# Kernel tuning notes

Measured on AMD Instinct MI355X. Metric: run time of the kernel, lower is better.

Reference implementation:

```python
import jax, jax.numpy as jnp
import numpy as np

D_MODEL = 1024
N_HEADS = 16
D_LATENT = 64
LN_EPS = 1e-5


def setup_inputs() -> dict:
    key = jax.random.key(0)
    ks = jax.random.split(key, 9)
    dm, h, dl = D_MODEL, N_HEADS, D_LATENT
    hd = h * dl
    # xavier_uniform with gain=0.1: limit = 0.1 * sqrt(6/(fan_in+fan_out))
    def xavier(k, fan_in, fan_out):
        lim = 0.1 * np.sqrt(6.0 / (fan_in + fan_out))
        return jax.random.uniform(k, (fan_in, fan_out), jnp.float32, -lim, lim)
    return {
        "x": jax.random.normal(ks[0], (4, 2048, dm), jnp.float32),
        "ln_g": jnp.ones((dm,), jnp.float32),
        "ln_b": jnp.zeros((dm,), jnp.float32),
        "wq": xavier(ks[1], dm, hd), "bq": jnp.zeros((hd,), jnp.float32),
        "wk": xavier(ks[2], dm, hd), "bk": jnp.zeros((hd,), jnp.float32),
        "wv": xavier(ks[3], dm, hd), "bv": jnp.zeros((hd,), jnp.float32),
        "wo": xavier(ks[4], hd, dm), "bo": jnp.zeros((dm,), jnp.float32),
    }


def reference(x, ln_g, ln_b, wq, bq, wk, bk, wv, bv, wo, bo):
    b, s, dm = x.shape
    h, dl = N_HEADS, D_LATENT
    # context = raw x (bound before LayerNorm in the torch code)
    context = x
    mu = jnp.mean(x, axis=-1, keepdims=True)
    var = jnp.var(x, axis=-1, keepdims=True)
    xn = (x - mu) * jax.lax.rsqrt(var + LN_EPS) * ln_g + ln_b
    q = (xn @ wq + bq).reshape(b, s, h, dl).transpose(0, 2, 1, 3)          # b h s d
    k = (context @ wk + bk).reshape(b, -1, h, dl).transpose(0, 2, 1, 3)    # b h t d
    v = (context @ wv + bv).reshape(b, -1, h, dl).transpose(0, 2, 1, 3)
    scores = jnp.einsum("bhsd,bhtd->bhst", q, k) / jnp.sqrt(jnp.float32(dl))
    attn = jax.nn.softmax(scores.astype(jnp.float32), axis=-1)
    # dropout omitted (eval mode / deterministic reference)
    out = jnp.einsum("bhst,bhtd->bhsd", attn, v)
    out = out.transpose(0, 2, 1, 3).reshape(b, s, h * dl)
    return out @ wo + bo
```

## Files before the change

### kernel.cpp

```cpp
#include <hip/hip_runtime.h>
#include <cstdint>

typedef __attribute__((ext_vector_type(8))) __bf16 bf16x8;
typedef __attribute__((ext_vector_type(8))) unsigned short u16x8;
typedef __attribute__((ext_vector_type(4))) unsigned short u16x4;
typedef __attribute__((ext_vector_type(4))) float f32x4;
typedef __attribute__((ext_vector_type(2))) unsigned int u32x2;
typedef __attribute__((ext_vector_type(4))) unsigned int u32x4;

__device__ inline unsigned short f2bf(float f) {
  return __builtin_bit_cast(unsigned short, (__bf16)f);
}

__device__ inline void llds16(const void* g, void* l) {
  __builtin_amdgcn_global_load_lds((const uint32_t*)g, (uint32_t*)l, 16, 0, 0);
}

__device__ inline bf16x8 ldfrag(const unsigned short* p) {
  u16x8 v = *(const u16x8*)p;
  return __builtin_bit_cast(bf16x8, v);
}

__device__ inline f32x4 mfma16(bf16x8 a, bf16x8 b, f32x4 c) {
  return __builtin_amdgcn_mfma_f32_16x16x32_bf16(a, b, c, 0, 0, 0);
}

__global__ __launch_bounds__(256) void ln_kernel(
    const float* __restrict__ x, const float* __restrict__ g, const float* __restrict__ be,
    unsigned short* __restrict__ xn, unsigned short* __restrict__ xb)
{
  const int row = blockIdx.x, tid = threadIdx.x;
  const size_t base = (size_t)row * 1024 + tid * 4;
  float4 v = *(const float4*)&x[base];
  float s  = v.x + v.y + v.z + v.w;
  float sq = v.x*v.x + v.y*v.y + v.z*v.z + v.w*v.w;
#pragma unroll
  for (int o = 1; o < 64; o <<= 1) { s += __shfl_xor(s, o); sq += __shfl_xor(sq, o); }
  __shared__ float ls[8];
  if ((tid & 63) == 0) { ls[tid >> 6] = s; ls[4 + (tid >> 6)] = sq; }
  __syncthreads();
  s  = ls[0] + ls[1] + ls[2] + ls[3];
  sq = ls[4] + ls[5] + ls[6] + ls[7];
  const float mu   = s * (1.f / 1024.f);
  const float var  = sq * (1.f / 1024.f) - mu * mu;
  const float rstd = rsqrtf(var + 1e-5f);
  float4 gv = *(const float4*)&g[tid * 4];
  float4 bv = *(const float4*)&be[tid * 4];
  u16x4 a, bb;
  a[0] = f2bf((v.x - mu) * rstd * gv.x + bv.x);
  a[1] = f2bf((v.y - mu) * rstd * gv.y + bv.y);
  a[2] = f2bf((v.z - mu) * rstd * gv.z + bv.z);
  a[3] = f2bf((v.w - mu) * rstd * gv.w + bv.w);
  bb[0] = f2bf(v.x); bb[1] = f2bf(v.y); bb[2] = f2bf(v.z); bb[3] = f2bf(v.w);
  *(u16x4*)&xn[base] = a;
  *(u16x4*)&xb[base] = bb;
}

__global__ __launch_bounds__(256) void wcast_kernel(
    const float* __restrict__ wq, const float* __restrict__ wk,
    const float* __restrict__ wv, const float* __restrict__ wo,
    unsigned short* __restrict__ wT, unsigned short* __restrict__ woT)
{
  __shared__ float t[64][66];
  const int z = blockIdx.z;
  const float* W = (z == 0) ? wq : (z == 1) ? wk : (z == 2) ? wv : wo;
  unsigned short* O = (z < 3) ? (wT + (size_t)z * 1048576) : woT;
  const int n0 = blockIdx.x * 64, k0 = blockIdx.y * 64;
  for (int idx = threadIdx.x; idx < 4096; idx += 256) {
    int r = idx >> 6, c = idx & 63;
    t[r][c] = W[(size_t)(k0 + r) * 1024 + n0 + c];
  }
  __syncthreads();
  for (int idx = threadIdx.x; idx < 4096; idx += 256) {
    int r = idx >> 6, c = idx & 63;
    O[(size_t)(n0 + r) * 1024 + k0 + c] = f2bf(t[c][r]);
  }
}

__global__ __launch_bounds__(256) void vtrans_kernel(
    const unsigned short* __restrict__ V, unsigned short* __restrict__ VT)
{
  __shared__ unsigned short t[64][66];
  const int bh = blockIdx.y, t0 = blockIdx.x * 64;
  const unsigned short* src = V + (size_t)bh * 131072 + (size_t)t0 * 64;
  for (int idx = threadIdx.x; idx < 4096; idx += 256) {
    int r = idx >> 6, c = idx & 63;
    t[r][c] = src[(size_t)r * 64 + c];
  }
  __syncthreads();
  unsigned short* dst = VT + (size_t)bh * 131072 + t0;
  for (int idx = threadIdx.x; idx < 4096; idx += 256) {
    int r = idx >> 6, c = idx & 63;
    dst[(size_t)r * 2048 + c] = t[c][r];
  }
}

template<int MODE>
__global__ __launch_bounds__(256) void gemm_kernel(
    const unsigned short* __restrict__ A0, const unsigned short* __restrict__ A1,
    const unsigned short* __restrict__ BT,
    const float* __restrict__ b0, const float* __restrict__ b1, const float* __restrict__ b2,
    void* __restrict__ Cv, int M, int N, int K)
{
  __shared__ unsigned short As[8192];
  __shared__ unsigned short Bs[8192];
  const int tid = threadIdx.x;
  const int wave = tid >> 6, lane = tid & 63;
  const int l15 = lane & 15, l4 = lane >> 4;
  const int swz = (l15 & 7) << 3;
  const int bn = blockIdx.x, bm = blockIdx.y;
  const int m0 = bm * 128, n0 = bn * 128;
  const unsigned short* Ap = (MODE == 0 && bn >= 8) ? A1 : A0;
  const int wr = (wave >> 1) * 64, wc = (wave & 1) * 64;

  f32x4 acc[4][4];
#pragma unroll
  for (int m = 0; m < 4; m++)
#pragma unroll
    for (int n = 0; n < 4; n++) acc[m][n] = {0.f, 0.f, 0.f, 0.f};

  for (int kt = 0; kt < K; kt += 64) {
    __syncthreads();
#pragma unroll
    for (int r = 0; r < 4; r++) {
      int D = r * 4096 + tid * 16;
      int row = D >> 7;
      int colus = ((D & 127) >> 1) ^ ((row & 7) << 3);
      llds16(&Ap[(size_t)(m0 + row) * K + kt + colus], &As[(r * 4096 + wave * 1024) >> 1]);
      llds16(&BT[(size_t)(n0 + row) * K + kt + colus], &Bs[(r * 4096 + wave * 1024) >> 1]);
    }
    __syncthreads();
#pragma unroll
    for (int ks = 0; ks < 2; ks++) {
      bf16x8 af[4], bfr[4];
#pragma unroll
      for (int m = 0; m < 4; m++)
        af[m]  = ldfrag(&As[(wr + m * 16 + l15) * 64 + ((ks * 32 + l4 * 8) ^ swz)]);
#pragma unroll
      for (int n = 0; n < 4; n++)
        bfr[n] = ldfrag(&Bs[(wc + n * 16 + l15) * 64 + ((ks * 32 + l4 * 8) ^ swz)]);
#pragma unroll
      for (int m = 0; m < 4; m++)
#pragma unroll
        for (int n = 0; n < 4; n++)
          acc[m][n] = mfma16(af[m], bfr[n], acc[m][n]);
    }
  }

#pragma unroll
  for (int nf = 0; nf < 4; nf++) {
    int c = n0 + wc + nf * 16 + l15;
    float bias; float sc = 1.0f;
    if (MODE == 0) {
      int sec = c >> 10;
      bias = (sec == 0 ? b0 : (sec == 1 ? b1 : b2))[c & 1023];
      if (sec == 0) sc = 0.18033688011112042f;
    } else {
      bias = b0[c];
    }
#pragma unroll
    for (int mf = 0; mf < 4; mf++) {
#pragma unroll
      for (int reg = 0; reg < 4; reg++) {
        int rrow = m0 + wr + mf * 16 + l4 * 4 + reg;
        float v = acc[mf][nf][reg] + bias;
        if (MODE == 0) {
          int sec = c >> 10, h = (c >> 6) & 15, d = c & 63;
          int b = rrow >> 11, t = rrow & 2047;
          ((unsigned short*)Cv)[(size_t)sec * 8388608 +
                                ((size_t)(b * 16 + h) * 2048 + t) * 64 + d] = f2bf(v * sc);
        } else {
          ((float*)Cv)[(size_t)rrow * N + c] = v;
        }
      }
    }
  }
}

__global__ __launch_bounds__(512, 4) void attn_kernel(
    const unsigned short* __restrict__ Q,
    const unsigned short* __restrict__ Kg,
    const unsigned short* __restrict__ VTg,
    unsigned short* __restrict__ Oa)
{
  __shared__ unsigned short S[32768];
  const int tid = threadIdx.x;
  const int wave = tid >> 6, lane = tid & 63;
  const int l15 = lane & 15, l4 = lane >> 4;
  const int swz = (l15 & 7) << 3;
  const int orig = blockIdx.x;
  const int wg = ((orig & 7) << 6) + (orig >> 3);
  const int qb = wg & 7, bh = wg >> 3;
  const size_t bhbase = (size_t)bh * 131072;
  const int q0 = qb * 256 + wave * 32;

  bf16x8 qf[2][2];
#pragma unroll
  for (int m = 0; m < 2; m++)
#pragma unroll
    for (int ks = 0; ks < 2; ks++)
      qf[m][ks] = ldfrag(&Q[bhbase + (size_t)(q0 + m * 16 + l15) * 64 + ks * 32 + l4 * 8]);

  f32x4 accO[2][4];
#pragma unroll
  for (int m = 0; m < 2; m++)
#pragma unroll
    for (int n = 0; n < 4; n++) accO[m][n] = {0.f, 0.f, 0.f, 0.f};
  float rowsum[2] = {0.f, 0.f};

  auto STAGE = [&](int b, int jj) {
#pragma unroll
    for (int r = 0; r < 2; r++) {
      int D = r * 8192 + tid * 16;
      int rowK = D >> 7;
      int colKus = ((D & 127) >> 1) ^ ((rowK & 7) << 3);
      llds16(&Kg[bhbase + (size_t)(jj * 128 + rowK) * 64 + colKus],
             &S[b * 16384 + r * 4096 + wave * 512]);
      int rowV = D >> 8;
      int colVus = ((D & 255) >> 1) ^ ((rowV & 7) << 3);
      llds16(&VTg[bhbase + (size_t)rowV * 2048 + jj * 128 + colVus],
             &S[b * 16384 + 8192 + r * 4096 + wave * 512]);
    }
  };

  int cur = 0;
  STAGE(0, 0);
  for (int j = 0; j < 16; j++) {
    if (j < 15) {
      STAGE(cur ^ 1, j + 1);
      asm volatile("s_waitcnt vmcnt(4)" ::: "memory");
    } else {
      asm volatile("s_waitcnt vmcnt(0)" ::: "memory");
    }
    __builtin_amdgcn_s_barrier();
    __builtin_amdgcn_sched_barrier(0);

    const unsigned short* Kb = &S[cur * 16384];
    const unsigned short* Vb = &S[cur * 16384 + 8192];

    float psum[2] = {0.f, 0.f};
#pragma unroll
    for (int kt = 0; kt < 4; kt++) {
      bf16x8 kf00 = ldfrag(&Kb[((2 * kt) * 16 + l15) * 64 + ((0 * 32 + l4 * 8) ^ swz)]);
      bf16x8 kf01 = ldfrag(&Kb[((2 * kt) * 16 + l15) * 64 + ((1 * 32 + l4 * 8) ^ swz)]);
      bf16x8 kf10 = ldfrag(&Kb[((2 * kt + 1) * 16 + l15) * 64 + ((0 * 32 + l4 * 8) ^ swz)]);
      bf16x8 kf11 = ldfrag(&Kb[((2 * kt + 1) * 16 + l15) * 64 + ((1 * 32 + l4 * 8) ^ swz)]);
      f32x4 sa = {0.f, 0.f, 0.f, 0.f}, sb = sa, sc = sa, sd = sa;
      __builtin_amdgcn_s_setprio(1);
      sa = mfma16(kf00, qf[0][0], sa); sb = mfma16(kf00, qf[1][0], sb);
      sc = mfma16(kf10, qf[0][0], sc); sd = mfma16(kf10, qf[1][0], sd);
      sa = mfma16(kf01, qf[0][1], sa); sb = mfma16(kf01, qf[1][1], sb);
      sc = mfma16(kf11, qf[0][1], sc); sd = mfma16(kf11, qf[1][1], sd);
      __builtin_amdgcn_s_setprio(0);

      bf16x8 vf[4];
#pragma unroll
      for (int n = 0; n < 4; n++)
        vf[n] = ldfrag(&Vb[(n * 16 + l15) * 128 + ((kt * 32 + l4 * 8) ^ swz)]);

      bf16x8 pf[2];
#pragma unroll
      for (int m = 0; m < 2; m++) {
        const f32x4 se = (m == 0) ? sa : sb;
        const f32x4 so = (m == 0) ? sc : sd;
        uint32_t V0, V1, V2, V3;
        {
          u16x4 pk;
#pragma unroll
          for (int r = 0; r < 4; r++) {
            float p = __builtin_amdgcn_exp2f(se[r]);
            psum[m] += p;
            pk[r] = f2bf(p);
          }
          u32x2 w = __builtin_bit_cast(u32x2, pk);
          V0 = w[0]; V1 = w[1];
        }
        {
          u16x4 pk;
#pragma unroll
          for (int r = 0; r < 4; r++) {
            float p = __builtin_amdgcn_exp2f(so[r]);
            psum[m] += p;
            pk[r] = f2bf(p);
          }
          u32x2 w = __builtin_bit_cast(u32x2, pk);
          V2 = w[0]; V3 = w[1];
        }
        asm("s_nop 1\n\t"
            "v_permlane32_swap_b32 %0, %2\n\t"
            "v_permlane32_swap_b32 %1, %3\n\t"
            "v_permlane16_swap_b32 %0, %2\n\t"
            "v_permlane16_swap_b32 %1, %3"
            : "+v"(V0), "+v"(V1), "+v"(V2), "+v"(V3));
        u32x4 fw = {V0, V1, V2, V3};
        pf[m] = __builtin_bit_cast(bf16x8, fw);
      }

      __builtin_amdgcn_s_setprio(1);
#pragma unroll
      for (int m = 0; m < 2; m++)
#pragma unroll
        for (int n = 0; n < 4; n++)
          accO[m][n] = mfma16(pf[m], vf[n], accO[m][n]);
      __builtin_amdgcn_s_setprio(0);
    }
#pragma unroll
    for (int m = 0; m < 2; m++) {
      float s = psum[m];
      s += __shfl_xor(s, 16);
      s += __shfl_xor(s, 32);
      rowsum[m] += s;
    }

    __builtin_amdgcn_s_barrier();
    cur ^= 1;
  }

  const int b = bh >> 4, h = bh & 15;
#pragma unroll
  for (int m = 0; m < 2; m++)
#pragma unroll
    for (int reg = 0; reg < 4; reg++) {
      float rs = __shfl(rowsum[m], l4 * 4 + reg);
      float inv = 1.0f / rs;
      int srow = q0 + m * 16 + l4 * 4 + reg;
#pragma unroll
      for (int n = 0; n < 4; n++) {
        float v = accO[m][n][reg] * inv;
        Oa[((size_t)(b * 2048) + srow) * 1024 + h * 64 + n * 16 + l15] = f2bf(v);
      }
    }
}

extern "C" void kernel_launch(void* const* d_in, const int* in_sizes, int n_in,
                              void* d_out, int out_size, void* d_ws, size_t ws_size,
                              hipStream_t stream) {
  (void)in_sizes; (void)n_in; (void)out_size; (void)ws_size;
  const float* x   = (const float*)d_in[0];
  const float* lng = (const float*)d_in[1];
  const float* lnb = (const float*)d_in[2];
  const float* wq  = (const float*)d_in[3];
  const float* bq  = (const float*)d_in[4];
  const float* wk  = (const float*)d_in[5];
  const float* bk  = (const float*)d_in[6];
  const float* wv  = (const float*)d_in[7];
  const float* bv  = (const float*)d_in[8];
  const float* wo  = (const float*)d_in[9];
  const float* bo  = (const float*)d_in[10];

  unsigned short* ws = (unsigned short*)d_ws;
  const size_t NE = 8388608;
  unsigned short* xn  = ws;
  unsigned short* xb  = ws + NE;
  unsigned short* wT  = ws + 2 * NE;
  unsigned short* woT = wT + 3145728;
  unsigned short* qkv = woT + 1048576;
  unsigned short* vT  = xn;
  unsigned short* oat = xb;

  wcast_kernel<<<dim3(16, 16, 4), 256, 0, stream>>>(wq, wk, wv, wo, wT, woT);
  ln_kernel<<<dim3(8192), 256, 0, stream>>>(x, lng, lnb, xn, xb);
  gemm_kernel<0><<<dim3(24, 64), 256, 0, stream>>>(xn, xb, wT, bq, bk, bv, qkv, 8192, 3072, 1024);
  vtrans_kernel<<<dim3(32, 64), 256, 0, stream>>>(qkv + 2 * NE, vT);
  attn_kernel<<<dim3(512), 512, 0, stream>>>(qkv, qkv + NE, vT, oat);
  gemm_kernel<1><<<dim3(8, 64), 256, 0, stream>>>(oat, oat, woT, bo, bo, bo, d_out, 8192, 1024, 1024);
}
```

Measured before the change: 200.1 us.

## Double-buffer GEMM LDS tiles and remap blocks for XCD locality

The GEMM kernel now uses two LDS buffers and issues the global-to-LDS loads for the next K tile before computing on the current one. Partial vmcnt waits let memory latency overlap with MFMA work. Launches switch to a 1D grid whose block IDs are remapped so that neighbouring tiles land on the same XCD, aiming for better L2 reuse. LDS per block doubles to 64KB, which can limit how many blocks fit per CU.

```diff
diff --git a/kernel.cpp b/kernel.cpp
--- a/kernel.cpp
+++ b/kernel.cpp
@@ -102,13 +102,16 @@
     const float* __restrict__ b0, const float* __restrict__ b1, const float* __restrict__ b2,
     void* __restrict__ Cv, int M, int N, int K)
 {
-  __shared__ unsigned short As[8192];
-  __shared__ unsigned short Bs[8192];
+  __shared__ unsigned short S[32768];
   const int tid = threadIdx.x;
   const int wave = tid >> 6, lane = tid & 63;
   const int l15 = lane & 15, l4 = lane >> 4;
   const int swz = (l15 & 7) << 3;
-  const int bn = blockIdx.x, bm = blockIdx.y;
+  const int NBN = N >> 7;
+  const int nwg = gridDim.x, cpx = nwg >> 3;
+  const int orig = blockIdx.x;
+  const int id = (orig & 7) * cpx + (orig >> 3);
+  const int bn = id % NBN, bm = id / NBN;
   const int m0 = bm * 128, n0 = bn * 128;
   const unsigned short* Ap = (MODE == 0 && bn >= 8) ? A1 : A0;
   const int wr = (wave >> 1) * 64, wc = (wave & 1) * 64;
@@ -119,32 +122,49 @@
 #pragma unroll
     for (int n = 0; n < 4; n++) acc[m][n] = {0.f, 0.f, 0.f, 0.f};
 
-  for (int kt = 0; kt < K; kt += 64) {
-    __syncthreads();
+  auto STAGE = [&](int b, int kt) {
 #pragma unroll
     for (int r = 0; r < 4; r++) {
       int D = r * 4096 + tid * 16;
       int row = D >> 7;
       int colus = ((D & 127) >> 1) ^ ((row & 7) << 3);
-      llds16(&Ap[(size_t)(m0 + row) * K + kt + colus], &As[(r * 4096 + wave * 1024) >> 1]);
-      llds16(&BT[(size_t)(n0 + row) * K + kt + colus], &Bs[(r * 4096 + wave * 1024) >> 1]);
-    }
-    __syncthreads();
+      llds16(&Ap[(size_t)(m0 + row) * K + kt + colus], &S[b * 16384 + r * 2048 + wave * 512]);
+      llds16(&BT[(size_t)(n0 + row) * K + kt + colus],
+             &S[b * 16384 + 8192 + r * 2048 + wave * 512]);
+    }
+  };
+
+  const int KSTEPS = K >> 6;
+  int cur = 0;
+  STAGE(0, 0);
+  for (int ki = 0; ki < KSTEPS; ki++) {
+    if (ki < KSTEPS - 1) {
+      STAGE(cur ^ 1, (ki + 1) << 6);
+      asm volatile("s_waitcnt vmcnt(8)" ::: "memory");
+    } else {
+      asm volatile("s_waitcnt vmcnt(0)" ::: "memory");
+    }
+    __builtin_amdgcn_s_barrier();
+    __builtin_amdgcn_sched_barrier(0);
+    const unsigned short* Asb = &S[cur * 16384];
+    const unsigned short* Bsb = &S[cur * 16384 + 8192];
 #pragma unroll
     for (int ks = 0; ks < 2; ks++) {
       bf16x8 af[4], bfr[4];
 #pragma unroll
       for (int m = 0; m < 4; m++)
-        af[m]  = ldfrag(&As[(wr + m * 16 + l15) * 64 + ((ks * 32 + l4 * 8) ^ swz)]);
+        af[m]  = ldfrag(&Asb[(wr + m * 16 + l15) * 64 + ((ks * 32 + l4 * 8) ^ swz)]);
 #pragma unroll
       for (int n = 0; n < 4; n++)
-        bfr[n] = ldfrag(&Bs[(wc + n * 16 + l15) * 64 + ((ks * 32 + l4 * 8) ^ swz)]);
+        bfr[n] = ldfrag(&Bsb[(wc + n * 16 + l15) * 64 + ((ks * 32 + l4 * 8) ^ swz)]);
 #pragma unroll
       for (int m = 0; m < 4; m++)
 #pragma unroll
         for (int n = 0; n < 4; n++)
           acc[m][n] = mfma16(af[m], bfr[n], acc[m][n]);
     }
+    __builtin_amdgcn_s_barrier();
+    cur ^= 1;
   }
 
 #pragma unroll
@@ -360,8 +380,8 @@
 
   wcast_kernel<<<dim3(16, 16, 4), 256, 0, stream>>>(wq, wk, wv, wo, wT, woT);
   ln_kernel<<<dim3(8192), 256, 0, stream>>>(x, lng, lnb, xn, xb);
-  gemm_kernel<0><<<dim3(24, 64), 256, 0, stream>>>(xn, xb, wT, bq, bk, bv, qkv, 8192, 3072, 1024);
+  gemm_kernel<0><<<dim3(1536), 256, 0, stream>>>(xn, xb, wT, bq, bk, bv, qkv, 8192, 3072, 1024);
   vtrans_kernel<<<dim3(32, 64), 256, 0, stream>>>(qkv + 2 * NE, vT);
   attn_kernel<<<dim3(512), 512, 0, stream>>>(qkv, qkv + NE, vT, oat);
-  gemm_kernel<1><<<dim3(8, 64), 256, 0, stream>>>(oat, oat, woT, bo, bo, bo, d_out, 8192, 1024, 1024);
-}
+  gemm_kernel<1><<<dim3(512), 256, 0, stream>>>(oat, oat, woT, bo, bo, bo, d_out, 8192, 1024, 1024);
+}
```

New measurement: 189.4 us. 1.06x faster.
